# Kernel tuning notes

Measured on AMD Instinct MI355X. Metric: run time of the kernel, lower is better.

## Reference

```python
import jax, jax.numpy as jnp
import numpy as np

B, D, U = 8192, 1024, 1024


def setup_inputs() -> dict:
    key = jax.random.key(0)
    ks = jax.random.split(key, 11)
    scale = 0.05  # keras 'random_normal' initializer default stddev
    inp = {
        "inputs": jax.random.normal(ks[0], (B, D), jnp.float32),
        "h_tm1": jax.random.normal(ks[1], (B, U), jnp.float32),
        "c_tm1": jax.random.normal(ks[2], (B, U), jnp.float32),
        "W_i": jax.random.normal(ks[3], (D, U), jnp.float32) * scale,
        "U_i": jax.random.normal(ks[4], (U, U), jnp.float32) * scale,
        "b_i": jnp.zeros((U,), jnp.float32),
        "W_f": jax.random.normal(ks[5], (D, U), jnp.float32) * scale,
        "U_f": jax.random.normal(ks[6], (U, U), jnp.float32) * scale,
        "b_f": jnp.zeros((U,), jnp.float32),
        "W_c": jax.random.normal(ks[7], (D, U), jnp.float32) * scale,
        "U_c": jax.random.normal(ks[8], (U, U), jnp.float32) * scale,
        "b_c": jnp.zeros((U,), jnp.float32),
        "W_o": jax.random.normal(ks[9], (D, U), jnp.float32) * scale,
        "U_o": jax.random.normal(ks[10], (U, U), jnp.float32) * scale,
        "b_o": jnp.zeros((U,), jnp.float32),
    }
    return inp


def reference(inputs, h_tm1, c_tm1, W_i, U_i, b_i, W_f, U_f, b_f, W_c, U_c, b_c, W_o, U_o, b_o):
    # Concatenate the 4 gate projections into single GEMMs (same math, fused form)
    Wx = jnp.concatenate([W_i, W_f, W_c, W_o], axis=1)  # [D, 4U]
    Uh = jnp.concatenate([U_i, U_f, U_c, U_o], axis=1)  # [U, 4U]
    b = jnp.concatenate([b_i, b_f, b_c, b_o], axis=0)   # [4U]
    z = inputs @ Wx + h_tm1 @ Uh + b                     # [B, 4U]
    u = W_i.shape[1]
    zi, zf, zc, zo = z[:, :u], z[:, u:2 * u], z[:, 2 * u:3 * u], z[:, 3 * u:]
    i = jax.nn.sigmoid(zi)
    f = jax.nn.sigmoid(zf)
    c_ = jnp.tanh(zc)
    c = f * c_tm1 + i * c_
    o = jax.nn.sigmoid(zo)
    h = o * jnp.tanh(c)
    return (h, c)
```

## Files before the change

### kernel.cpp

```cpp
#include <hip/hip_runtime.h>
#include <hip/hip_bf16.h>
#include <cstdint>


using f32x4  = __attribute__((ext_vector_type(4))) float;
using short8 = __attribute__((ext_vector_type(8))) short;

__device__ __forceinline__ unsigned short f2bf(float f) {
  union { float f; unsigned int u; } v; v.f = f;
  unsigned int r = v.u + 0x7fffu + ((v.u >> 16) & 1u);
  return (unsigned short)(r >> 16);
}
__device__ __forceinline__ float sigmoidf_fast(float x) { return 1.f / (1.f + __expf(-x)); }
__device__ __forceinline__ float tanhf_fast(float x)    { return 1.f - 2.f / (__expf(2.f * x) + 1.f); }

__global__ void conv_a_kernel(const float* __restrict__ X, const float* __restrict__ H,
                              unsigned short* __restrict__ Abf) {
  int idx = blockIdx.x * blockDim.x + threadIdx.x;
  int b  = idx >> 8;
  int kq = (idx & 255) << 2;
  float4 x = *(const float4*)(X + (long)b * 1024 + kq);
  float4 h = *(const float4*)(H + (long)b * 1024 + kq);
  ushort4 xo, ho;
  xo.x = f2bf(x.x); xo.y = f2bf(x.y); xo.z = f2bf(x.z); xo.w = f2bf(x.w);
  ho.x = f2bf(h.x); ho.y = f2bf(h.y); ho.z = f2bf(h.z); ho.w = f2bf(h.w);
  *(ushort4*)(Abf + (long)b * 2048 + kq)        = xo;
  *(ushort4*)(Abf + (long)b * 2048 + 1024 + kq) = ho;
}

__global__ void conv_b_kernel(const float* W_i, const float* U_i,
                              const float* W_f, const float* U_f,
                              const float* W_c, const float* U_c,
                              const float* W_o, const float* U_o,
                              unsigned short* __restrict__ Bt) {
  __shared__ float tile[64][65];
  int z = blockIdx.z;
  const float* src;
  switch (z) {
    case 0: src = W_i; break; case 1: src = U_i; break;
    case 2: src = W_f; break; case 3: src = U_f; break;
    case 4: src = W_c; break; case 5: src = U_c; break;
    case 6: src = W_o; break; default: src = U_o; break;
  }
  int g = z >> 1, s = z & 1;
  int k0 = blockIdx.x * 64;
  int u0 = blockIdx.y * 64;
  int t = threadIdx.x;
  int c = t & 63, r0 = t >> 6;
#pragma unroll
  for (int i = 0; i < 16; ++i) {
    int r = i * 4 + r0;
    tile[r][c] = src[(long)(k0 + r) * 1024 + u0 + c];
  }
  __syncthreads();
  int ul = t >> 2;
  int ks = (t & 3) * 16;
  unsigned short outv[16];
#pragma unroll
  for (int j = 0; j < 16; ++j) outv[j] = f2bf(tile[ks + j][ul]);
  long n   = 4L * u0 + (ul >> 4) * 64 + g * 16 + (ul & 15);
  long col = (long)s * 1024 + k0 + ks;
  uint4* dst = (uint4*)(Bt + n * 2048 + col);
  dst[0] = *(uint4*)(outv);
  dst[1] = *(uint4*)(outv + 8);
}

__global__ __launch_bounds__(512, 4) void lstm_gemm_kernel(
    const unsigned short* __restrict__ Abf,
    const unsigned short* __restrict__ Btbf,
    const float* __restrict__ b_i, const float* __restrict__ b_f,
    const float* __restrict__ b_c, const float* __restrict__ b_o,
    const float* __restrict__ c_tm1,
    float* __restrict__ outH, float* __restrict__ outC) {
  __shared__ unsigned short smem[3 * 12288];

  int bid = blockIdx.x;
  int swz = (bid & 7) * 128 + (bid >> 3);
  int bm = swz >> 5;
  int bn = swz & 31;

  int t = threadIdx.x;
  int lane = t & 63;
  int w = t >> 6;
  int wm = w >> 1;
  int wn = w & 1;
  int rl = lane & 15;
  int kg = lane >> 4;

#define AOFFE(MI) (((wm * 64 + (MI) * 16 + rl) * 32) + \
    ((kg ^ (((wm * 64 + (MI) * 16 + rl) >> 1) & 3)) << 3))
#define BOFFE(NI) (8192 + ((wn * 64 + (NI) * 16 + rl) * 32) + \
    ((kg ^ (((wn * 64 + (NI) * 16 + rl) >> 1) & 3)) << 3))
  const int offA0 = AOFFE(0), offA1 = AOFFE(1), offA2 = AOFFE(2), offA3 = AOFFE(3);
  const int offB0 = BOFFE(0), offB1 = BOFFE(1), offB2 = BOFFE(2), offB3 = BOFFE(3);
#undef AOFFE
#undef BOFFE

  int srow = t >> 2;
  int cbe  = ((t & 3) ^ ((srow >> 1) & 3)) << 3;
  const unsigned short* aS0 = Abf  + (long)(bm * 256 + srow) * 2048 + cbe;
  const unsigned short* aS1 = aS0 + 128L * 2048;
  const unsigned short* bS0 = Btbf + (long)(bn * 128 + srow) * 2048 + cbe;
  const int dA = t * 8;

#define GLL(SRC, DELM)                                                                     \
  __builtin_amdgcn_global_load_lds((const __attribute__((address_space(1))) void*)(SRC),   \
      (__attribute__((address_space(3))) void*)(&smem[DELM]), 16, 0, 0)
#define STAGE(SB, KOFF)                                                        \
  do {                                                                         \
    GLL(aS0 + (KOFF), (SB) * 12288 + dA);                                      \
    GLL(aS1 + (KOFF), (SB) * 12288 + 4096 + dA);                               \
    GLL(bS0 + (KOFF), (SB) * 12288 + 8192 + dA);                               \
  } while (0)
#define VMC(N) asm volatile("s_waitcnt vmcnt(" #N ")" ::: "memory")

  f32x4 acc[4][4];
#pragma unroll
  for (int mi = 0; mi < 4; ++mi)
#pragma unroll
    for (int ni = 0; ni < 4; ++ni) acc[mi][ni] = (f32x4){0.f, 0.f, 0.f, 0.f};

  short8 aw0, aw1, aw2, aw3, bb0, bb1, bb2, bb3;

#define MF4(AF, MI)                                                                      \
  acc[MI][0] = __builtin_amdgcn_mfma_f32_16x16x32_bf16(AF, bb0, acc[MI][0], 0, 0, 0);    \
  acc[MI][1] = __builtin_amdgcn_mfma_f32_16x16x32_bf16(AF, bb1, acc[MI][1], 0, 0, 0);    \
  acc[MI][2] = __builtin_amdgcn_mfma_f32_16x16x32_bf16(AF, bb2, acc[MI][2], 0, 0, 0);    \
  acc[MI][3] = __builtin_amdgcn_mfma_f32_16x16x32_bf16(AF, bb3, acc[MI][3], 0, 0, 0);

#define WINDOW(RB, SB, KOFF, DOSTAGE, VMN, DOBAR)                              \
  {                                                                            \
    const unsigned short* S_ = smem + (RB) * 12288;                            \
    bb0 = *(const short8*)(S_ + offB0);                                        \
    bb1 = *(const short8*)(S_ + offB1);                                        \
    bb2 = *(const short8*)(S_ + offB2);                                        \
    bb3 = *(const short8*)(S_ + offB3);                                        \
    aw0 = *(const short8*)(S_ + offA0);                                        \
    aw1 = *(const short8*)(S_ + offA1);                                        \
    aw2 = *(const short8*)(S_ + offA2);                                        \
    aw3 = *(const short8*)(S_ + offA3);                                        \
    if (DOSTAGE) STAGE(SB, KOFF);                                              \
    __builtin_amdgcn_s_setprio(1);                                             \
    MF4(aw0, 0) MF4(aw1, 1) MF4(aw2, 2) MF4(aw3, 3)                            \
    __builtin_amdgcn_s_setprio(0);                                             \
    if ((VMN) == 3) VMC(3);                                                    \
    if ((VMN) == 0) VMC(0);                                                    \
    if (DOBAR) __builtin_amdgcn_s_barrier();                                   \
  }

  STAGE(0, 0);
  STAGE(1, 32);
  VMC(3);
  __builtin_amdgcn_s_barrier();
  aS0 += 64; aS1 += 64; bS0 += 64;

  for (int g = 0; g < 20; ++g) {
    WINDOW(0, 2, 0,  1, 3, 1);
    WINDOW(1, 0, 32, 1, 3, 1);
    WINDOW(2, 1, 64, 1, 3, 1);
    aS0 += 96; aS1 += 96; bS0 += 96;
  }
  WINDOW(0, 2, 0,  1, 3, 1);
  WINDOW(1, 0, 32, 1, 3, 1);
  WINDOW(2, 0, 0,  0, 0, 1);
  WINDOW(0, 0, 0,  0, -1, 0);
#undef WINDOW
#undef MF4
#undef VMC
#undef STAGE
#undef GLL

  int mbase = bm * 256 + wm * 64;
  int nbase = bn * 128 + wn * 64;
  int u = (nbase >> 2) + rl;
  float bi_v = b_i[u], bf_v = b_f[u], bc_v = b_c[u], bo_v = b_o[u];
  int rquad = (lane >> 4) << 2;
#pragma unroll
  for (int mi = 0; mi < 4; ++mi) {
#pragma unroll
    for (int j = 0; j < 4; ++j) {
      int brow = mbase + mi * 16 + rquad + j;
      float zi = acc[mi][0][j] + bi_v;
      float zf = acc[mi][1][j] + bf_v;
      float zc = acc[mi][2][j] + bc_v;
      float zo = acc[mi][3][j] + bo_v;
      float ig = sigmoidf_fast(zi);
      float fg = sigmoidf_fast(zf);
      float cg = tanhf_fast(zc);
      float og = sigmoidf_fast(zo);
      float cp = c_tm1[(long)brow * 1024 + u];
      float cn = fg * cp + ig * cg;
      float hn = og * tanhf_fast(cn);
      outH[(long)brow * 1024 + u] = hn;
      outC[(long)brow * 1024 + u] = cn;
    }
  }
}

extern "C" void kernel_launch(void* const* d_in, const int* in_sizes, int n_in,
                              void* d_out, int out_size, void* d_ws, size_t ws_size,
                              hipStream_t stream) {
  (void)in_sizes; (void)n_in; (void)out_size; (void)ws_size;
  const float* X   = (const float*)d_in[0];
  const float* Hst = (const float*)d_in[1];
  const float* Cst = (const float*)d_in[2];
  const float* W_i = (const float*)d_in[3];
  const float* U_i = (const float*)d_in[4];
  const float* b_i = (const float*)d_in[5];
  const float* W_f = (const float*)d_in[6];
  const float* U_f = (const float*)d_in[7];
  const float* b_f = (const float*)d_in[8];
  const float* W_c = (const float*)d_in[9];
  const float* U_c = (const float*)d_in[10];
  const float* b_c = (const float*)d_in[11];
  const float* W_o = (const float*)d_in[12];
  const float* U_o = (const float*)d_in[13];
  const float* b_o = (const float*)d_in[14];

  unsigned short* Abf  = (unsigned short*)d_ws;
  unsigned short* Btbf = (unsigned short*)((char*)d_ws + 33554432);

  float* outH = (float*)d_out;
  float* outC = outH + 8192L * 1024;

  conv_a_kernel<<<8192, 256, 0, stream>>>(X, Hst, Abf);
  conv_b_kernel<<<dim3(16, 16, 8), 256, 0, stream>>>(W_i, U_i, W_f, U_f, W_c, U_c, W_o, U_o, Btbf);
  lstm_gemm_kernel<<<1024, 512, 0, stream>>>(Abf, Btbf, b_i, b_f, b_c, b_o, Cst, outH, outC);
}
```

Measured before the change: 174.3 us.

## Deepen LDS ring to five stages and barrier once per two K-windows

The GEMM main loop moves from a three-buffer LDS ring with a barrier after every 32-wide K window to a five-buffer ring. The prologue preloads three stages, and the loop waits and synchronises once per pair of windows. Launch bounds drop to two waves-per-EU to match the larger shared-memory footprint. The aim is to hide global-load latency and cut barrier overhead, at the cost of roughly 120 KB of LDS per block and fewer resident blocks per CU.

```diff
diff --git a/kernel.cpp b/kernel.cpp
--- a/kernel.cpp
+++ b/kernel.cpp
@@ -65,14 +65,14 @@
   dst[1] = *(uint4*)(outv + 8);
 }
 
-__global__ __launch_bounds__(512, 4) void lstm_gemm_kernel(
+__global__ __launch_bounds__(512, 2) void lstm_gemm_kernel(
     const unsigned short* __restrict__ Abf,
     const unsigned short* __restrict__ Btbf,
     const float* __restrict__ b_i, const float* __restrict__ b_f,
     const float* __restrict__ b_c, const float* __restrict__ b_o,
     const float* __restrict__ c_tm1,
     float* __restrict__ outH, float* __restrict__ outC) {
-  __shared__ unsigned short smem[3 * 12288];
+  __shared__ unsigned short smem[5 * 12288];
 
   int bid = blockIdx.x;
   int swz = (bid & 7) * 128 + (bid >> 3);
@@ -113,6 +113,11 @@
     GLL(bS0 + (KOFF), (SB) * 12288 + 8192 + dA);                               \
   } while (0)
 #define VMC(N) asm volatile("s_waitcnt vmcnt(" #N ")" ::: "memory")
+#define BARS()                                                                 \
+  do {                                                                         \
+    __builtin_amdgcn_s_barrier();                                              \
+    __builtin_amdgcn_sched_barrier(0);                                         \
+  } while (0)
 
   f32x4 acc[4][4];
 #pragma unroll
@@ -128,7 +133,7 @@
   acc[MI][2] = __builtin_amdgcn_mfma_f32_16x16x32_bf16(AF, bb2, acc[MI][2], 0, 0, 0);    \
   acc[MI][3] = __builtin_amdgcn_mfma_f32_16x16x32_bf16(AF, bb3, acc[MI][3], 0, 0, 0);
 
-#define WINDOW(RB, SB, KOFF, DOSTAGE, VMN, DOBAR)                              \
+#define WINDOW(RB, SB, KOFF, DOST)                                             \
   {                                                                            \
     const unsigned short* S_ = smem + (RB) * 12288;                            \
     bb0 = *(const short8*)(S_ + offB0);                                        \
@@ -139,33 +144,35 @@
     aw1 = *(const short8*)(S_ + offA1);                                        \
     aw2 = *(const short8*)(S_ + offA2);                                        \
     aw3 = *(const short8*)(S_ + offA3);                                        \
-    if (DOSTAGE) STAGE(SB, KOFF);                                              \
+    if (DOST) STAGE(SB, KOFF);                                                 \
     __builtin_amdgcn_s_setprio(1);                                             \
     MF4(aw0, 0) MF4(aw1, 1) MF4(aw2, 2) MF4(aw3, 3)                            \
     __builtin_amdgcn_s_setprio(0);                                             \
-    if ((VMN) == 3) VMC(3);                                                    \
-    if ((VMN) == 0) VMC(0);                                                    \
-    if (DOBAR) __builtin_amdgcn_s_barrier();                                   \
   }
 
   STAGE(0, 0);
   STAGE(1, 32);
+  STAGE(2, 64);
   VMC(3);
-  __builtin_amdgcn_s_barrier();
-  aS0 += 64; aS1 += 64; bS0 += 64;
-
-  for (int g = 0; g < 20; ++g) {
-    WINDOW(0, 2, 0,  1, 3, 1);
-    WINDOW(1, 0, 32, 1, 3, 1);
-    WINDOW(2, 1, 64, 1, 3, 1);
-    aS0 += 96; aS1 += 96; bS0 += 96;
-  }
-  WINDOW(0, 2, 0,  1, 3, 1);
-  WINDOW(1, 0, 32, 1, 3, 1);
-  WINDOW(2, 0, 0,  0, 0, 1);
-  WINDOW(0, 0, 0,  0, -1, 0);
+  BARS();
+
+  for (int g = 0; g < 6; ++g) {
+    WINDOW(0, 3, 96,  1) WINDOW(1, 4, 128, 1) VMC(3); BARS();
+    WINDOW(2, 0, 160, 1) WINDOW(3, 1, 192, 1) VMC(3); BARS();
+    WINDOW(4, 2, 224, 1) WINDOW(0, 3, 256, 1) VMC(3); BARS();
+    WINDOW(1, 4, 288, 1) WINDOW(2, 0, 320, 1) VMC(3); BARS();
+    WINDOW(3, 1, 352, 1) WINDOW(4, 2, 384, 1) VMC(3); BARS();
+    aS0 += 320; aS1 += 320; bS0 += 320;
+  }
+  WINDOW(0, 3, 96, 1)
+  WINDOW(1, 0, 0, 0)
+  VMC(0);
+  BARS();
+  WINDOW(2, 0, 0, 0)
+  WINDOW(3, 0, 0, 0)
 #undef WINDOW
 #undef MF4
+#undef BARS
 #undef VMC
 #undef STAGE
 #undef GLL
```

New measurement: 183.7 us. 1.05x slower.

## Enlarge GEMM block tile to 256x256 with 128x128 per-wave register tiles

Applied to the files above, without the earlier changes.

The fused LSTM GEMM block tile grows from 256x128 with eight waves to 256x256 with four waves, each wave computing a 128x128 sub-tile held in an 8x8 accumulator array. This raises MFMA work per LDS fragment load and cuts global/LDS traffic per FLOP. A-fragment loads are software-pipelined between MFMA groups, with scheduling barriers to keep that order. The cost is very high VGPR pressure, one wave per SIMD and larger LDS stages, which leaves less latency hiding. The grid is also halved to 512 blocks.

```diff
diff --git a/kernel.cpp b/kernel.cpp
--- a/kernel.cpp
+++ b/kernel.cpp
@@ -65,19 +65,19 @@
   dst[1] = *(uint4*)(outv + 8);
 }
 
-__global__ __launch_bounds__(512, 4) void lstm_gemm_kernel(
+__global__ __launch_bounds__(256, 1) void lstm_gemm_kernel(
     const unsigned short* __restrict__ Abf,
     const unsigned short* __restrict__ Btbf,
     const float* __restrict__ b_i, const float* __restrict__ b_f,
     const float* __restrict__ b_c, const float* __restrict__ b_o,
     const float* __restrict__ c_tm1,
     float* __restrict__ outH, float* __restrict__ outC) {
-  __shared__ unsigned short smem[3 * 12288];
+  __shared__ unsigned short smem[49152];
 
   int bid = blockIdx.x;
-  int swz = (bid & 7) * 128 + (bid >> 3);
-  int bm = swz >> 5;
-  int bn = swz & 31;
+  int swz = (bid & 7) * 64 + (bid >> 3);
+  int bm = swz >> 4;
+  int bn = swz & 15;
 
   int t = threadIdx.x;
   int lane = t & 63;
@@ -87,112 +87,150 @@
   int rl = lane & 15;
   int kg = lane >> 4;
 
-#define AOFFE(MI) (((wm * 64 + (MI) * 16 + rl) * 32) + \
-    ((kg ^ (((wm * 64 + (MI) * 16 + rl) >> 1) & 3)) << 3))
-#define BOFFE(NI) (8192 + ((wn * 64 + (NI) * 16 + rl) * 32) + \
-    ((kg ^ (((wn * 64 + (NI) * 16 + rl) >> 1) & 3)) << 3))
+#define AOFFE(MI) ((wm * 128 + (MI) * 16 + rl) * 32 + \
+    ((kg ^ (((wm * 128 + (MI) * 16 + rl) >> 1) & 3)) << 3))
+#define BOFFE(NI) (8192 + (wn * 128 + (NI) * 16 + rl) * 32 + \
+    ((kg ^ (((wn * 128 + (NI) * 16 + rl) >> 1) & 3)) << 3))
   const int offA0 = AOFFE(0), offA1 = AOFFE(1), offA2 = AOFFE(2), offA3 = AOFFE(3);
+  const int offA4 = AOFFE(4), offA5 = AOFFE(5), offA6 = AOFFE(6), offA7 = AOFFE(7);
   const int offB0 = BOFFE(0), offB1 = BOFFE(1), offB2 = BOFFE(2), offB3 = BOFFE(3);
+  const int offB4 = BOFFE(4), offB5 = BOFFE(5), offB6 = BOFFE(6), offB7 = BOFFE(7);
 #undef AOFFE
 #undef BOFFE
 
-  int srow = t >> 2;
-  int cbe  = ((t & 3) ^ ((srow >> 1) & 3)) << 3;
-  const unsigned short* aS0 = Abf  + (long)(bm * 256 + srow) * 2048 + cbe;
-  const unsigned short* aS1 = aS0 + 128L * 2048;
-  const unsigned short* bS0 = Btbf + (long)(bn * 128 + srow) * 2048 + cbe;
-  const int dA = t * 8;
+  int cbe = (((t & 3) ^ ((t >> 3) & 3))) << 3;
+  const unsigned short* aS = Abf  + (long)(bm * 256 + (t >> 2)) * 2048 + cbe;
+  const unsigned short* bS = Btbf + (long)(bn * 256 + (t >> 2)) * 2048 + cbe;
+  const int dT = t * 8;
 
 #define GLL(SRC, DELM)                                                                     \
   __builtin_amdgcn_global_load_lds((const __attribute__((address_space(1))) void*)(SRC),   \
       (__attribute__((address_space(3))) void*)(&smem[DELM]), 16, 0, 0)
 #define STAGE(SB, KOFF)                                                        \
   do {                                                                         \
-    GLL(aS0 + (KOFF), (SB) * 12288 + dA);                                      \
-    GLL(aS1 + (KOFF), (SB) * 12288 + 4096 + dA);                               \
-    GLL(bS0 + (KOFF), (SB) * 12288 + 8192 + dA);                               \
+    GLL(aS + (KOFF),          (SB) * 16384 + dT);                              \
+    GLL(aS + 131072 + (KOFF), (SB) * 16384 + 2048 + dT);                       \
+    GLL(aS + 262144 + (KOFF), (SB) * 16384 + 4096 + dT);                       \
+    GLL(aS + 393216 + (KOFF), (SB) * 16384 + 6144 + dT);                       \
+    GLL(bS + (KOFF),          (SB) * 16384 + 8192 + dT);                       \
+    GLL(bS + 131072 + (KOFF), (SB) * 16384 + 10240 + dT);                      \
+    GLL(bS + 262144 + (KOFF), (SB) * 16384 + 12288 + dT);                      \
+    GLL(bS + 393216 + (KOFF), (SB) * 16384 + 14336 + dT);                      \
   } while (0)
 #define VMC(N) asm volatile("s_waitcnt vmcnt(" #N ")" ::: "memory")
-
-  f32x4 acc[4][4];
-#pragma unroll
-  for (int mi = 0; mi < 4; ++mi)
-#pragma unroll
-    for (int ni = 0; ni < 4; ++ni) acc[mi][ni] = (f32x4){0.f, 0.f, 0.f, 0.f};
-
-  short8 aw0, aw1, aw2, aw3, bb0, bb1, bb2, bb3;
-
-#define MF4(AF, MI)                                                                      \
+#define SB0()  __builtin_amdgcn_sched_barrier(0)
+
+  f32x4 acc[8][8];
+#pragma unroll
+  for (int mi = 0; mi < 8; ++mi)
+#pragma unroll
+    for (int ni = 0; ni < 8; ++ni) acc[mi][ni] = (f32x4){0.f, 0.f, 0.f, 0.f};
+
+  short8 aX, aY, bb0, bb1, bb2, bb3, bb4, bb5, bb6, bb7;
+
+#define MFG(AF, MI)                                                                      \
   acc[MI][0] = __builtin_amdgcn_mfma_f32_16x16x32_bf16(AF, bb0, acc[MI][0], 0, 0, 0);    \
   acc[MI][1] = __builtin_amdgcn_mfma_f32_16x16x32_bf16(AF, bb1, acc[MI][1], 0, 0, 0);    \
   acc[MI][2] = __builtin_amdgcn_mfma_f32_16x16x32_bf16(AF, bb2, acc[MI][2], 0, 0, 0);    \
-  acc[MI][3] = __builtin_amdgcn_mfma_f32_16x16x32_bf16(AF, bb3, acc[MI][3], 0, 0, 0);
-
-#define WINDOW(RB, SB, KOFF, DOSTAGE, VMN, DOBAR)                              \
+  acc[MI][3] = __builtin_amdgcn_mfma_f32_16x16x32_bf16(AF, bb3, acc[MI][3], 0, 0, 0);    \
+  acc[MI][4] = __builtin_amdgcn_mfma_f32_16x16x32_bf16(AF, bb4, acc[MI][4], 0, 0, 0);    \
+  acc[MI][5] = __builtin_amdgcn_mfma_f32_16x16x32_bf16(AF, bb5, acc[MI][5], 0, 0, 0);    \
+  acc[MI][6] = __builtin_amdgcn_mfma_f32_16x16x32_bf16(AF, bb6, acc[MI][6], 0, 0, 0);    \
+  acc[MI][7] = __builtin_amdgcn_mfma_f32_16x16x32_bf16(AF, bb7, acc[MI][7], 0, 0, 0);
+
+#define WINDOW(RB, SB, KOFF, DOST, VMN, DOBAR)                                 \
   {                                                                            \
-    const unsigned short* S_ = smem + (RB) * 12288;                            \
+    const unsigned short* S_ = smem + (RB) * 16384;                            \
     bb0 = *(const short8*)(S_ + offB0);                                        \
     bb1 = *(const short8*)(S_ + offB1);                                        \
     bb2 = *(const short8*)(S_ + offB2);                                        \
     bb3 = *(const short8*)(S_ + offB3);                                        \
-    aw0 = *(const short8*)(S_ + offA0);                                        \
-    aw1 = *(const short8*)(S_ + offA1);                                        \
-    aw2 = *(const short8*)(S_ + offA2);                                        \
-    aw3 = *(const short8*)(S_ + offA3);                                        \
-    if (DOSTAGE) STAGE(SB, KOFF);                                              \
-    __builtin_amdgcn_s_setprio(1);                                             \
-    MF4(aw0, 0) MF4(aw1, 1) MF4(aw2, 2) MF4(aw3, 3)                            \
-    __builtin_amdgcn_s_setprio(0);                                             \
-    if ((VMN) == 3) VMC(3);                                                    \
+    bb4 = *(const short8*)(S_ + offB4);                                        \
+    bb5 = *(const short8*)(S_ + offB5);                                        \
+    bb6 = *(const short8*)(S_ + offB6);                                        \
+    bb7 = *(const short8*)(S_ + offB7);                                        \
+    aX  = *(const short8*)(S_ + offA0);                                        \
+    if (DOST) STAGE(SB, KOFF);                                                 \
+    SB0();                                                                     \
+    aY = *(const short8*)(S_ + offA1); MFG(aX, 0) SB0();                       \
+    aX = *(const short8*)(S_ + offA2); MFG(aY, 1) SB0();                       \
+    aY = *(const short8*)(S_ + offA3); MFG(aX, 2) SB0();                       \
+    aX = *(const short8*)(S_ + offA4); MFG(aY, 3) SB0();                       \
+    aY = *(const short8*)(S_ + offA5); MFG(aX, 4) SB0();                       \
+    aX = *(const short8*)(S_ + offA6); MFG(aY, 5) SB0();                       \
+    aY = *(const short8*)(S_ + offA7); MFG(aX, 6) SB0();                       \
+    MFG(aY, 7)                                                                 \
+    if ((VMN) == 8) VMC(8);                                                    \
     if ((VMN) == 0) VMC(0);                                                    \
     if (DOBAR) __builtin_amdgcn_s_barrier();                                   \
   }
 
   STAGE(0, 0);
   STAGE(1, 32);
-  VMC(3);
+  VMC(8);
   __builtin_amdgcn_s_barrier();
-  aS0 += 64; aS1 += 64; bS0 += 64;
+  aS += 64; bS += 64;
 
   for (int g = 0; g < 20; ++g) {
-    WINDOW(0, 2, 0,  1, 3, 1);
-    WINDOW(1, 0, 32, 1, 3, 1);
-    WINDOW(2, 1, 64, 1, 3, 1);
-    aS0 += 96; aS1 += 96; bS0 += 96;
-  }
-  WINDOW(0, 2, 0,  1, 3, 1);
-  WINDOW(1, 0, 32, 1, 3, 1);
+    WINDOW(0, 2, 0,  1, 8, 1);
+    WINDOW(1, 0, 32, 1, 8, 1);
+    WINDOW(2, 1, 64, 1, 8, 1);
+    aS += 96; bS += 96;
+  }
+  WINDOW(0, 2, 0,  1, 8, 1);
+  WINDOW(1, 0, 32, 1, 8, 1);
   WINDOW(2, 0, 0,  0, 0, 1);
   WINDOW(0, 0, 0,  0, -1, 0);
 #undef WINDOW
-#undef MF4
+#undef MFG
+#undef SB0
 #undef VMC
 #undef STAGE
 #undef GLL
 
-  int mbase = bm * 256 + wm * 64;
-  int nbase = bn * 128 + wn * 64;
-  int u = (nbase >> 2) + rl;
-  float bi_v = b_i[u], bf_v = b_f[u], bc_v = b_c[u], bo_v = b_o[u];
-  int rquad = (lane >> 4) << 2;
-#pragma unroll
-  for (int mi = 0; mi < 4; ++mi) {
+  int mbase = bm * 256 + wm * 128;
+  int nbase = bn * 256 + wn * 128;
+  int ub = nbase >> 2;
+  int u0 = ub + rl;
+  int u1 = ub + 16 + rl;
+  float bi0 = b_i[u0], bf0 = b_f[u0], bc0 = b_c[u0], bo0 = b_o[u0];
+  float bi1 = b_i[u1], bf1 = b_f[u1], bc1 = b_c[u1], bo1 = b_o[u1];
+  int rquad = kg << 2;
+#pragma unroll
+  for (int mi = 0; mi < 8; ++mi) {
 #pragma unroll
     for (int j = 0; j < 4; ++j) {
       int brow = mbase + mi * 16 + rquad + j;
-      float zi = acc[mi][0][j] + bi_v;
-      float zf = acc[mi][1][j] + bf_v;
-      float zc = acc[mi][2][j] + bc_v;
-      float zo = acc[mi][3][j] + bo_v;
-      float ig = sigmoidf_fast(zi);
-      float fg = sigmoidf_fast(zf);
-      float cg = tanhf_fast(zc);
-      float og = sigmoidf_fast(zo);
-      float cp = c_tm1[(long)brow * 1024 + u];
-      float cn = fg * cp + ig * cg;
-      float hn = og * tanhf_fast(cn);
-      outH[(long)brow * 1024 + u] = hn;
-      outC[(long)brow * 1024 + u] = cn;
+      {
+        float zi = acc[mi][0][j] + bi0;
+        float zf = acc[mi][1][j] + bf0;
+        float zc = acc[mi][2][j] + bc0;
+        float zo = acc[mi][3][j] + bo0;
+        float ig = sigmoidf_fast(zi);
+        float fg = sigmoidf_fast(zf);
+        float cg = tanhf_fast(zc);
+        float og = sigmoidf_fast(zo);
+        float cp = c_tm1[(long)brow * 1024 + u0];
+        float cn = fg * cp + ig * cg;
+        float hn = og * tanhf_fast(cn);
+        outH[(long)brow * 1024 + u0] = hn;
+        outC[(long)brow * 1024 + u0] = cn;
+      }
+      {
+        float zi = acc[mi][4][j] + bi1;
+        float zf = acc[mi][5][j] + bf1;
+        float zc = acc[mi][6][j] + bc1;
+        float zo = acc[mi][7][j] + bo1;
+        float ig = sigmoidf_fast(zi);
+        float fg = sigmoidf_fast(zf);
+        float cg = tanhf_fast(zc);
+        float og = sigmoidf_fast(zo);
+        float cp = c_tm1[(long)brow * 1024 + u1];
+        float cn = fg * cp + ig * cg;
+        float hn = og * tanhf_fast(cn);
+        outH[(long)brow * 1024 + u1] = hn;
+        outC[(long)brow * 1024 + u1] = cn;
+      }
     }
   }
 }
@@ -225,5 +263,5 @@
 
   conv_a_kernel<<<8192, 256, 0, stream>>>(X, Hst, Abf);
   conv_b_kernel<<<dim3(16, 16, 8), 256, 0, stream>>>(W_i, U_i, W_f, U_f, W_c, U_c, W_o, U_o, Btbf);
-  lstm_gemm_kernel<<<1024, 512, 0, stream>>>(Abf, Btbf, b_i, b_f, b_c, b_o, Cst, outH, outC);
-}
+  lstm_gemm_kernel<<<512, 256, 0, stream>>>(Abf, Btbf, b_i, b_f, b_c, b_o, Cst, outH, outC);
+}
```

Result: slower. 201.6 us (+15.7%).
